# Kernel optimization log

Hardware: AMD Instinct MI355X
Metric: run time of the kernel (lower is better)

The kernel has to match this reference:

```python
import jax, jax.numpy as jnp
import numpy as np

NUM_HEADS = 16
HEAD_DIM = 128
VALUE_HEAD_DIM = 128
CHUNK = 1024
ROPE_BASE = 10000.0


def _rope(q, k, start):
    # q, k: (B, T, H, D). Rotate pairs (first half, second half) per RotaryEmbedding.
    B, T, H, D = q.shape
    half = D // 2
    inv_freq = jnp.exp(jnp.arange(half, dtype=jnp.float32) * (-np.log(ROPE_BASE) / half))
    pos = jnp.arange(T, dtype=jnp.float32) + jnp.float32(start)
    ang = pos[:, None] * inv_freq[None, :]            # (T, half)
    cos = jnp.cos(ang)[None, :, None, :].astype(q.dtype)
    sin = jnp.sin(ang)[None, :, None, :].astype(q.dtype)

    def rot(x):
        a, b = jnp.split(x, 2, axis=-1)
        return jnp.concatenate([a * cos - b * sin, b * cos + a * sin], axis=-1)

    return rot(q), rot(k)


def setup_inputs() -> dict:
    key = jax.random.key(0)
    k1, k2, k3 = jax.random.split(key, 3)
    B, L = 4, 4096
    q = jax.random.normal(k1, (B, L, NUM_HEADS, HEAD_DIM), dtype=jnp.float32)
    k = jax.random.normal(k2, (B, L, NUM_HEADS, HEAD_DIM), dtype=jnp.float32)
    v = jax.random.normal(k3, (B, L, NUM_HEADS, VALUE_HEAD_DIM), dtype=jnp.float32)
    return {"q": q, "k": k, "v": v, "start_index": 0}


def reference(q, k, v, start_index):
    # ChunkedSelfAttention.forward with cache=None, attn_mask=None, training=False:
    # RoPE at absolute positions, then causal SDPA within each chunk of size CHUNK.
    B, L, H, Dh = q.shape
    Dv = v.shape[-1]
    q, k = _rope(q, k, start_index)
    nc = L // CHUNK
    qc = q.reshape(B, nc, CHUNK, H, Dh)
    kc = k.reshape(B, nc, CHUNK, H, Dh)
    vc = v.reshape(B, nc, CHUNK, H, Dv)
    scale = 1.0 / np.sqrt(Dh).astype(np.float32)
    scores = jnp.einsum('bnqhd,bnkhd->bnhqk', qc, kc) * scale  # (B, nc, H, C, C)
    i = jnp.arange(CHUNK)
    causal = i[:, None] >= i[None, :]                          # (C, C)
    neg = jnp.asarray(jnp.finfo(scores.dtype).min, scores.dtype)
    scores = jnp.where(causal[None, None, None], scores, neg)
    attn = jax.nn.softmax(scores, axis=-1)
    out = jnp.einsum('bnhqk,bnkhd->bnqhd', attn, vc)
    return out.reshape(B, L, H, Dv)
```

## Files before the change

kernel.cpp:

```cpp
#include <hip/hip_runtime.h>


typedef __attribute__((ext_vector_type(2)))  float     f32x2;
typedef __attribute__((ext_vector_type(4)))  float     f32x4;
typedef __attribute__((ext_vector_type(16))) float     f32x16;
typedef __attribute__((ext_vector_type(8)))  _Float16  f16x8;
typedef unsigned int   u32;
typedef unsigned short u16;
typedef __attribute__((ext_vector_type(4))) unsigned int u32x4;

#define MFMA(a, b, c) __builtin_amdgcn_mfma_f32_32x32x16_f16(a, b, c, 0, 0, 0)

constexpr int Ll = 4096;
constexpr float QSCALE = 0.08838834764831845f * 1.4426950408889634f;

#define KSTR 66
#define VSTR 34
#define KBUF (64 * KSTR)
#define VBUF (128 * VSTR)
#define STG  (KBUF + VBUF)

__device__ __forceinline__ f32x4 ld_f32x4(const void* p) { f32x4 v; __builtin_memcpy(&v, p, 16); return v; }
__device__ __forceinline__ f32x2 ld_f32x2(const void* p) { f32x2 v; __builtin_memcpy(&v, p, 8);  return v; }
__device__ __forceinline__ f16x8 ld_frag(const u32* dwp) {
  f16x8 v;
  __builtin_memcpy(&v, dwp, 8);
  __builtin_memcpy(((char*)&v) + 8, dwp + 2, 8);
  return v;
}

__device__ __forceinline__ u32 packh(_Float16 a, _Float16 b) {
  return (u32)__builtin_bit_cast(u16, a) | ((u32)__builtin_bit_cast(u16, b) << 16);
}

__global__ void rope_table_k(const int* __restrict__ startp, float* __restrict__ tab) {
  int idx = blockIdx.x * 256 + threadIdx.x;
  int t = idx >> 6, hid = idx & 63;
  float a = (float)hid * (-0.14391156831212878f);
  float invf = expf(a);
  float ang = (float)(t + startp[0]) * invf;
  tab[2 * idx]     = cosf(ang);
  tab[2 * idx + 1] = sinf(ang);
}

__global__ __launch_bounds__(512, 2)
void chunked_attn_k(const float* __restrict__ Qg, const float* __restrict__ Kg,
                    const float* __restrict__ Vg, float* __restrict__ Og,
                    const float* __restrict__ tab) {
  __shared__ __align__(16) u32 lds[2 * STG];

  const int bx  = blockIdx.x;
  const int h   = bx & 15;
  const int p   = (bx >> 4) & 1;
  const int c   = (bx >> 5) & 3;
  const int b   = bx >> 7;
  const int tid = threadIdx.x;
  const int w   = tid >> 6;
  const int lane= tid & 63;
  const int l31 = lane & 31;
  const int lg2 = lane >> 5;

  const size_t cbase = (size_t)(b * Ll + c * 1024);
  const size_t hoff  = (size_t)h * 128;
  const int tb = c * 1024;

  f32x2 pk[8], pva[4], pvb[4];

  auto issue = [&](int j) {
    const float* kb_ = Kg + (cbase + (size_t)j * 64) * 2048 + hoff;
    const float* vb_ = Vg + (cbase + (size_t)j * 64) * 2048 + hoff;
    #pragma unroll
    for (int r = 0; r < 8; ++r)
      pk[r] = ld_f32x2(kb_ + (size_t)(8 * w + r) * 2048 + 2 * lane);
    #pragma unroll
    for (int rp = 0; rp < 4; ++rp) {
      const float* vr = vb_ + (size_t)(8 * w + 2 * rp) * 2048 + 2 * lane;
      pva[rp] = ld_f32x2(vr);
      pvb[rp] = ld_f32x2(vr + 2048);
    }
  };

  auto xform = [&](int j, int s) {
    u32* KB = lds + s * STG;
    u32* VB = KB + KBUF;
    const float* tbase = tab + (size_t)(tb + j * 64) * 128 + 4 * l31;
    f32x4 cs[8];
    #pragma unroll
    for (int r = 0; r < 8; ++r)
      cs[r] = ld_f32x4(tbase + (size_t)(8 * w + r) * 128);
    const float sgn = (lane < 32) ? -1.0f : 1.0f;
    #pragma unroll
    for (int r = 0; r < 8; ++r) {
      float a0 = pk[r].x, a1 = pk[r].y;
      float p0 = __shfl_xor(a0, 32), p1 = __shfl_xor(a1, 32);
      float o0 = a0 * cs[r].x + sgn * (p0 * cs[r].y);
      float o1 = a1 * cs[r].z + sgn * (p1 * cs[r].w);
      KB[(8 * w + r) * KSTR + lane] = packh((_Float16)o0, (_Float16)o1);
    }
    #pragma unroll
    for (int rp = 0; rp < 4; ++rp) {
      int kp = 4 * w + rp;
      VB[(2 * lane) * VSTR + kp]     = packh((_Float16)pva[rp].x, (_Float16)pvb[rp].x);
      VB[(2 * lane + 1) * VSTR + kp] = packh((_Float16)pva[rp].y, (_Float16)pvb[rp].y);
    }
  };

  #pragma unroll 1
  for (int sp = 0; sp < 2; ++sp) {
    const int qs = sp ? p : (3 - p);
    const int qrow = qs * 256 + w * 32 + l31;

    const float* qbase = Qg + (cbase + qrow) * 2048 + hoff;
    float xq[8][8];
    #pragma unroll
    for (int ds = 0; ds < 8; ++ds) {
      const float* ptr = qbase + ds * 16 + lg2 * 8;
      f32x4 v0 = ld_f32x4(ptr);
      f32x4 v1 = ld_f32x4(ptr + 4);
      xq[ds][0]=v0.x; xq[ds][1]=v0.y; xq[ds][2]=v0.z; xq[ds][3]=v0.w;
      xq[ds][4]=v1.x; xq[ds][5]=v1.y; xq[ds][6]=v1.z; xq[ds][7]=v1.w;
    }
    const float* trowq = tab + (size_t)(tb + qrow) * 128 + lg2 * 16;
    #pragma unroll
    for (int ds = 0; ds < 4; ++ds) {
      #pragma unroll
      for (int i2 = 0; i2 < 4; ++i2) {
        f32x4 cs = ld_f32x4(trowq + ds * 32 + i2 * 4);
        int i0 = 2 * i2;
        float a0 = xq[ds][i0],     b0 = xq[ds + 4][i0];
        xq[ds][i0]     = a0 * cs.x - b0 * cs.y;
        xq[ds + 4][i0] = b0 * cs.x + a0 * cs.y;
        float a1 = xq[ds][i0 + 1], b1 = xq[ds + 4][i0 + 1];
        xq[ds][i0 + 1]     = a1 * cs.z - b1 * cs.w;
        xq[ds + 4][i0 + 1] = b1 * cs.z + a1 * cs.w;
      }
    }
    f16x8 qh[8];
    #pragma unroll
    for (int ds = 0; ds < 8; ++ds)
      #pragma unroll
      for (int i = 0; i < 8; ++i)
        qh[ds][i] = (_Float16)(xq[ds][i] * QSCALE);

    f32x16 O[4];
    #pragma unroll
    for (int n = 0; n < 4; ++n) O[n] = (f32x16)0.0f;
    float m2 = -1e30f, lsum = 0.0f;
    const int  nt    = 4 * (qs + 1);
    const int  jmaxw = 4 * qs + (w >> 1);
    const bool oddw  = w & 1;

    issue(0);
    xform(0, 0);
    __syncthreads();

    for (int j = 0; j < nt; ++j) {
      const int s = j & 1;
      const bool more = (j + 1 < nt);
      if (more) issue(j + 1);

      if (j <= jmaxw) {
        const bool full = oddw || (j < jmaxw);
        const u32* KB = lds + s * STG;
        const u32* VB = KB + KBUF;
        const u32* kr0 = KB + (size_t)l31 * KSTR + lg2 * 4;
        const u32* kr1 = kr0 + (size_t)32 * KSTR;

        f32x16 S0 = (f32x16)0.0f, S1 = (f32x16)0.0f;
        __builtin_amdgcn_s_setprio(1);
        #pragma unroll
        for (int ds = 0; ds < 8; ++ds) {
          S0 = MFMA(ld_frag(kr0 + ds * 8), qh[ds], S0);
          if (full) S1 = MFMA(ld_frag(kr1 + ds * 8), qh[ds], S1);
        }
        __builtin_amdgcn_s_setprio(0);

        if (j == jmaxw) {
          #pragma unroll
          for (int r = 0; r < 16; ++r) {
            int crow = (r & 3) + 8 * (r >> 2) + 4 * lg2;
            if (crow > l31) { if (oddw) S1[r] = -1e30f; else S0[r] = -1e30f; }
          }
        }

        float tm = S0[0];
        #pragma unroll
        for (int r = 1; r < 16; ++r) tm = fmaxf(tm, S0[r]);
        if (full) {
          #pragma unroll
          for (int r = 0; r < 16; ++r) tm = fmaxf(tm, S1[r]);
        }
        tm = fmaxf(tm, __shfl_xor(tm, 32));
        if (!__all(tm <= m2 + 8.0f)) {
          float m2n = fmaxf(m2, tm);
          float fac = exp2f(m2 - m2n);
          lsum *= fac;
          #pragma unroll
          for (int r = 0; r < 16; ++r) {
            int rq = (r & 3) + 8 * (r >> 2) + 4 * lg2;
            float fr = __shfl(fac, rq);
            O[0][r] *= fr; O[1][r] *= fr; O[2][r] *= fr; O[3][r] *= fr;
          }
          m2 = m2n;
        }
        u32 U[16];
        float ps = 0.0f;
        #pragma unroll
        for (int t = 0; t < 8; ++t) {
          float e0 = exp2f(S0[2 * t]     - m2);
          float e1 = exp2f(S0[2 * t + 1] - m2);
          U[t] = packh((_Float16)e0, (_Float16)e1);
          ps += e0 + e1;
        }
        if (full) {
          #pragma unroll
          for (int t = 0; t < 8; ++t) {
            float e0 = exp2f(S1[2 * t]     - m2);
            float e1 = exp2f(S1[2 * t + 1] - m2);
            U[8 + t] = packh((_Float16)e0, (_Float16)e1);
            ps += e0 + e1;
          }
        }
        ps += __shfl_xor(ps, 32);
        lsum += ps;

        __builtin_amdgcn_s_setprio(1);
        #pragma unroll
        for (int ks = 0; ks < 4; ++ks) {
          if (ks >= 2 && !full) continue;
          u32 a0 = U[4 * ks + 0], a1 = U[4 * ks + 1];
          u32 b0 = U[4 * ks + 2], b1 = U[4 * ks + 3];
          asm("v_permlane32_swap_b32 %0, %1" : "+v"(a0), "+v"(b0));
          asm("v_permlane32_swap_b32 %0, %1" : "+v"(a1), "+v"(b1));
          u32x4 t4; t4.x = a0; t4.y = a1; t4.z = b0; t4.w = b1;
          f16x8 pa = __builtin_bit_cast(f16x8, t4);
          #pragma unroll
          for (int n = 0; n < 4; ++n) {
            const u32* vp = VB + (size_t)(32 * n + l31) * VSTR + 8 * ks + 4 * lg2;
            O[n] = MFMA(pa, ld_frag(vp), O[n]);
          }
        }
        __builtin_amdgcn_s_setprio(0);
      }

      if (more) xform(j + 1, s ^ 1);
      __syncthreads();
    }

    float inv = 1.0f / lsum;
    #pragma unroll
    for (int r = 0; r < 16; ++r) {
      int rq = (r & 3) + 8 * (r >> 2) + 4 * lg2;
      float fi = __shfl(inv, rq);
      float* orow = Og + (cbase + qs * 256 + w * 32 + rq) * 2048 + hoff + l31;
      orow[0]  = O[0][r] * fi;
      orow[32] = O[1][r] * fi;
      orow[64] = O[2][r] * fi;
      orow[96] = O[3][r] * fi;
    }
  }
}

extern "C" void kernel_launch(void* const* d_in, const int* in_sizes, int n_in,
                              void* d_out, int out_size, void* d_ws, size_t ws_size,
                              hipStream_t stream) {
  const float* q = (const float*)d_in[0];
  const float* k = (const float*)d_in[1];
  const float* v = (const float*)d_in[2];
  const int* start = (const int*)d_in[3];
  float* out = (float*)d_out;
  float* tab = (float*)d_ws;

  rope_table_k<<<dim3(1024), dim3(256), 0, stream>>>(start, tab);
  chunked_attn_k<<<dim3(512), dim3(512), 0, stream>>>(q, k, v, out, tab);
}
```

Measured before the change: 315.7 us.

## Precompute RoPE'd fp16 K and transposed fp16 V in separate prep kernels

Adds two prepass kernels. One applies RoPE to K and converts it to fp16 in a swizzled per-chunk tile layout, and the other converts V to fp16 and transposes it into tiles. The attention kernel then streams these pre-formatted tiles straight into LDS with 16-byte copies and uses XOR swizzle addressing instead of padded strides. The aim is to halve K/V bytes read inside the main loop and remove per-tile rotary and transpose work that attention blocks repeat. In exchange it adds extra kernel launches and a full write and re-read of 128 MB of workspace, and it falls back to the old kernel if the workspace is too small.

```diff
diff --git a/kernel.cpp b/kernel.cpp
--- a/kernel.cpp
+++ b/kernel.cpp
@@ -14,21 +14,17 @@
 constexpr int Ll = 4096;
 constexpr float QSCALE = 0.08838834764831845f * 1.4426950408889634f;
 
-#define KSTR 66
-#define VSTR 34
-#define KBUF (64 * KSTR)
-#define VBUF (128 * VSTR)
-#define STG  (KBUF + VBUF)
-
 __device__ __forceinline__ f32x4 ld_f32x4(const void* p) { f32x4 v; __builtin_memcpy(&v, p, 16); return v; }
 __device__ __forceinline__ f32x2 ld_f32x2(const void* p) { f32x2 v; __builtin_memcpy(&v, p, 8);  return v; }
+__device__ __forceinline__ u32x4 ld_u32x4(const void* p) { u32x4 v; __builtin_memcpy(&v, p, 16); return v; }
+__device__ __forceinline__ void  st_u32x4(void* p, u32x4 v) { __builtin_memcpy(p, &v, 16); }
+__device__ __forceinline__ f16x8 ld_f16x8(const void* p) { f16x8 v; __builtin_memcpy(&v, p, 16); return v; }
 __device__ __forceinline__ f16x8 ld_frag(const u32* dwp) {
   f16x8 v;
   __builtin_memcpy(&v, dwp, 8);
   __builtin_memcpy(((char*)&v) + 8, dwp + 2, 8);
   return v;
 }
-
 __device__ __forceinline__ u32 packh(_Float16 a, _Float16 b) {
   return (u32)__builtin_bit_cast(u16, a) | ((u32)__builtin_bit_cast(u16, b) << 16);
 }
@@ -43,11 +39,67 @@
   tab[2 * idx + 1] = sinf(ang);
 }
 
+__global__ __launch_bounds__(256)
+void prep_k_kernel(const float* __restrict__ Kg, const float* __restrict__ tab,
+                   u32* __restrict__ Kh) {
+  const int R    = blockIdx.x * 4 + (threadIdx.x >> 6);
+  const int lane = threadIdx.x & 63;
+  const int h  = R & 15;
+  const int bt = R >> 4;
+  const int b  = bt >> 12;
+  const int t  = bt & 4095;
+  const int c  = t >> 10;
+  const int j  = (t >> 6) & 15;
+  const int row = t & 63;
+  const int GID = (b * 4 + c) * 16 + h;
+  const int sw  = (row & 7) << 4;
+  const int dc  = ((4 * lane) ^ sw) >> 1;
+  f32x2 a = ld_f32x2(Kg + (size_t)R * 128 + dc);
+  float p0 = __shfl_xor(a.x, 32);
+  float p1 = __shfl_xor(a.y, 32);
+  f32x4 cs = ld_f32x4(tab + (size_t)t * 128 + 2 * (dc & 63));
+  const float sgn = (dc < 64) ? -1.0f : 1.0f;
+  float o0 = a.x * cs.x + sgn * (p0 * cs.y);
+  float o1 = a.y * cs.z + sgn * (p1 * cs.w);
+  Kh[((size_t)(GID * 16 + j) * 64 + row) * 64 + lane] = packh((_Float16)o0, (_Float16)o1);
+}
+
+__global__ __launch_bounds__(256)
+void prep_vt_kernel(const float* __restrict__ Vg, u32* __restrict__ VT) {
+  __shared__ __align__(16) u32 tile[4096];
+  const int gj  = blockIdx.x;
+  const int GID = gj >> 4, j = gj & 15;
+  const int h = GID & 15, c = (GID >> 4) & 3, b = GID >> 6;
+  const int tid = threadIdx.x;
+  const size_t rowbase = ((size_t)(b * 4096 + c * 1024 + j * 64)) * 16 + h;
+  const int k  = tid >> 2;
+  const int dq = tid & 3;
+  u16* t16 = (u16*)tile;
+  #pragma unroll
+  for (int it = 0; it < 8; ++it) {
+    int dv0 = dq * 4 + 16 * it;
+    f32x4 v4 = ld_f32x4(Vg + (rowbase + (size_t)k * 16) * 128 + dv0);
+    #pragma unroll
+    for (int u = 0; u < 4; ++u) {
+      int dv = dv0 + u;
+      int ci = k ^ ((dv & 7) << 3);
+      t16[dv * 64 + ci] = __builtin_bit_cast(u16, (_Float16)v4[u]);
+    }
+  }
+  __syncthreads();
+  const u32* tsrc = tile + 16 * tid;
+  u32* dst = VT + (size_t)gj * 4096 + 16 * tid;
+  #pragma unroll
+  for (int u = 0; u < 4; ++u) st_u32x4(dst + 4 * u, ld_u32x4(tsrc + 4 * u));
+}
+
+#define ATT_STG 8192
+
 __global__ __launch_bounds__(512, 2)
-void chunked_attn_k(const float* __restrict__ Qg, const float* __restrict__ Kg,
-                    const float* __restrict__ Vg, float* __restrict__ Og,
-                    const float* __restrict__ tab) {
-  __shared__ __align__(16) u32 lds[2 * STG];
+void attn_f16_k(const float* __restrict__ Qg, const u32* __restrict__ Kh,
+                const u32* __restrict__ VT, float* __restrict__ Og,
+                const float* __restrict__ tab) {
+  __shared__ __align__(16) u32 lds[2 * ATT_STG];
 
   const int bx  = blockIdx.x;
   const int h   = bx & 15;
@@ -62,46 +114,27 @@
 
   const size_t cbase = (size_t)(b * Ll + c * 1024);
   const size_t hoff  = (size_t)h * 128;
-  const int tb = c * 1024;
-
-  f32x2 pk[8], pva[4], pvb[4];
-
+  const int tb  = c * 1024;
+  const int GID = (b * 4 + c) * 16 + h;
+  const u32* khg = Kh + (size_t)GID * 16 * 4096;
+  const u32* vtg = VT + (size_t)GID * 16 * 4096;
+
+  u32x4 stg[4];
   auto issue = [&](int j) {
-    const float* kb_ = Kg + (cbase + (size_t)j * 64) * 2048 + hoff;
-    const float* vb_ = Vg + (cbase + (size_t)j * 64) * 2048 + hoff;
-    #pragma unroll
-    for (int r = 0; r < 8; ++r)
-      pk[r] = ld_f32x2(kb_ + (size_t)(8 * w + r) * 2048 + 2 * lane);
-    #pragma unroll
-    for (int rp = 0; rp < 4; ++rp) {
-      const float* vr = vb_ + (size_t)(8 * w + 2 * rp) * 2048 + 2 * lane;
-      pva[rp] = ld_f32x2(vr);
-      pvb[rp] = ld_f32x2(vr + 2048);
+    #pragma unroll
+    for (int i = 0; i < 4; ++i) {
+      int ch = w + 8 * i;
+      const u32* src = (ch < 16) ? (khg + (size_t)j * 4096 + ch * 256 + 4 * lane)
+                                 : (vtg + (size_t)j * 4096 + (ch - 16) * 256 + 4 * lane);
+      stg[i] = ld_u32x4(src);
     }
   };
-
-  auto xform = [&](int j, int s) {
-    u32* KB = lds + s * STG;
-    u32* VB = KB + KBUF;
-    const float* tbase = tab + (size_t)(tb + j * 64) * 128 + 4 * l31;
-    f32x4 cs[8];
-    #pragma unroll
-    for (int r = 0; r < 8; ++r)
-      cs[r] = ld_f32x4(tbase + (size_t)(8 * w + r) * 128);
-    const float sgn = (lane < 32) ? -1.0f : 1.0f;
-    #pragma unroll
-    for (int r = 0; r < 8; ++r) {
-      float a0 = pk[r].x, a1 = pk[r].y;
-      float p0 = __shfl_xor(a0, 32), p1 = __shfl_xor(a1, 32);
-      float o0 = a0 * cs[r].x + sgn * (p0 * cs[r].y);
-      float o1 = a1 * cs[r].z + sgn * (p1 * cs[r].w);
-      KB[(8 * w + r) * KSTR + lane] = packh((_Float16)o0, (_Float16)o1);
-    }
-    #pragma unroll
-    for (int rp = 0; rp < 4; ++rp) {
-      int kp = 4 * w + rp;
-      VB[(2 * lane) * VSTR + kp]     = packh((_Float16)pva[rp].x, (_Float16)pvb[rp].x);
-      VB[(2 * lane + 1) * VSTR + kp] = packh((_Float16)pva[rp].y, (_Float16)pvb[rp].y);
+  auto store_stage = [&](int s) {
+    u32* dst0 = lds + (size_t)s * ATT_STG;
+    #pragma unroll
+    for (int i = 0; i < 4; ++i) {
+      int ch = w + 8 * i;
+      st_u32x4(dst0 + ch * 256 + 4 * lane, stg[i]);
     }
   };
 
@@ -151,7 +184,7 @@
     const bool oddw  = w & 1;
 
     issue(0);
-    xform(0, 0);
+    store_stage(0);
     __syncthreads();
 
     for (int j = 0; j < nt; ++j) {
@@ -161,17 +194,19 @@
 
       if (j <= jmaxw) {
         const bool full = oddw || (j < jmaxw);
-        const u32* KB = lds + s * STG;
-        const u32* VB = KB + KBUF;
-        const u32* kr0 = KB + (size_t)l31 * KSTR + lg2 * 4;
-        const u32* kr1 = kr0 + (size_t)32 * KSTR;
+        const u32* KB = lds + (size_t)s * ATT_STG;
+        const u32* VB = KB + 4096;
+        const u32* kr0 = KB + (size_t)l31 * 64;
+        const u32* kr1 = kr0 + 32 * 64;
+        const int  swk = (l31 & 7) << 2;
 
         f32x16 S0 = (f32x16)0.0f, S1 = (f32x16)0.0f;
         __builtin_amdgcn_s_setprio(1);
         #pragma unroll
         for (int ds = 0; ds < 8; ++ds) {
-          S0 = MFMA(ld_frag(kr0 + ds * 8), qh[ds], S0);
-          if (full) S1 = MFMA(ld_frag(kr1 + ds * 8), qh[ds], S1);
+          int dc = (8 * ds + 4 * lg2) ^ swk;
+          S0 = MFMA(ld_f16x8(kr0 + dc), qh[ds], S0);
+          if (full) S1 = MFMA(ld_f16x8(kr1 + dc), qh[ds], S1);
         }
         __builtin_amdgcn_s_setprio(0);
 
@@ -234,16 +269,16 @@
           asm("v_permlane32_swap_b32 %0, %1" : "+v"(a1), "+v"(b1));
           u32x4 t4; t4.x = a0; t4.y = a1; t4.z = b0; t4.w = b1;
           f16x8 pa = __builtin_bit_cast(f16x8, t4);
+          int dcv = (8 * ks + 4 * lg2) ^ swk;
           #pragma unroll
           for (int n = 0; n < 4; ++n) {
-            const u32* vp = VB + (size_t)(32 * n + l31) * VSTR + 8 * ks + 4 * lg2;
-            O[n] = MFMA(pa, ld_frag(vp), O[n]);
+            O[n] = MFMA(pa, ld_f16x8(VB + (size_t)(32 * n + l31) * 32 + dcv), O[n]);
           }
         }
         __builtin_amdgcn_s_setprio(0);
       }
 
-      if (more) xform(j + 1, s ^ 1);
+      if (more) store_stage(s ^ 1);
       __syncthreads();
     }
 
@@ -261,6 +296,230 @@
   }
 }
 
+#define KSTR 66
+#define VSTR 34
+#define KBUF (64 * KSTR)
+#define VBUF (128 * VSTR)
+#define STG  (KBUF + VBUF)
+
+__global__ __launch_bounds__(512, 2)
+void chunked_attn_fb(const float* __restrict__ Qg, const float* __restrict__ Kg,
+                     const float* __restrict__ Vg, float* __restrict__ Og,
+                     const float* __restrict__ tab) {
+  __shared__ __align__(16) u32 lds[2 * STG];
+
+  const int bx  = blockIdx.x;
+  const int h   = bx & 15;
+  const int p   = (bx >> 4) & 1;
+  const int c   = (bx >> 5) & 3;
+  const int b   = bx >> 7;
+  const int tid = threadIdx.x;
+  const int w   = tid >> 6;
+  const int lane= tid & 63;
+  const int l31 = lane & 31;
+  const int lg2 = lane >> 5;
+
+  const size_t cbase = (size_t)(b * Ll + c * 1024);
+  const size_t hoff  = (size_t)h * 128;
+  const int tb = c * 1024;
+
+  f32x2 pk[8], pva[4], pvb[4];
+
+  auto issue = [&](int j) {
+    const float* kb_ = Kg + (cbase + (size_t)j * 64) * 2048 + hoff;
+    const float* vb_ = Vg + (cbase + (size_t)j * 64) * 2048 + hoff;
+    #pragma unroll
+    for (int r = 0; r < 8; ++r)
+      pk[r] = ld_f32x2(kb_ + (size_t)(8 * w + r) * 2048 + 2 * lane);
+    #pragma unroll
+    for (int rp = 0; rp < 4; ++rp) {
+      const float* vr = vb_ + (size_t)(8 * w + 2 * rp) * 2048 + 2 * lane;
+      pva[rp] = ld_f32x2(vr);
+      pvb[rp] = ld_f32x2(vr + 2048);
+    }
+  };
+
+  auto xform = [&](int j, int s) {
+    u32* KB = lds + s * STG;
+    u32* VB = KB + KBUF;
+    const float* tbase = tab + (size_t)(tb + j * 64) * 128 + 4 * l31;
+    f32x4 cs[8];
+    #pragma unroll
+    for (int r = 0; r < 8; ++r)
+      cs[r] = ld_f32x4(tbase + (size_t)(8 * w + r) * 128);
+    const float sgn = (lane < 32) ? -1.0f : 1.0f;
+    #pragma unroll
+    for (int r = 0; r < 8; ++r) {
+      float a0 = pk[r].x, a1 = pk[r].y;
+      float p0 = __shfl_xor(a0, 32), p1 = __shfl_xor(a1, 32);
+      float o0 = a0 * cs[r].x + sgn * (p0 * cs[r].y);
+      float o1 = a1 * cs[r].z + sgn * (p1 * cs[r].w);
+      KB[(8 * w + r) * KSTR + lane] = packh((_Float16)o0, (_Float16)o1);
+    }
+    #pragma unroll
+    for (int rp = 0; rp < 4; ++rp) {
+      int kp = 4 * w + rp;
+      VB[(2 * lane) * VSTR + kp]     = packh((_Float16)pva[rp].x, (_Float16)pvb[rp].x);
+      VB[(2 * lane + 1) * VSTR + kp] = packh((_Float16)pva[rp].y, (_Float16)pvb[rp].y);
+    }
+  };
+
+  #pragma unroll 1
+  for (int sp = 0; sp < 2; ++sp) {
+    const int qs = sp ? p : (3 - p);
+    const int qrow = qs * 256 + w * 32 + l31;
+
+    const float* qbase = Qg + (cbase + qrow) * 2048 + hoff;
+    float xq[8][8];
+    #pragma unroll
+    for (int ds = 0; ds < 8; ++ds) {
+      const float* ptr = qbase + ds * 16 + lg2 * 8;
+      f32x4 v0 = ld_f32x4(ptr);
+      f32x4 v1 = ld_f32x4(ptr + 4);
+      xq[ds][0]=v0.x; xq[ds][1]=v0.y; xq[ds][2]=v0.z; xq[ds][3]=v0.w;
+      xq[ds][4]=v1.x; xq[ds][5]=v1.y; xq[ds][6]=v1.z; xq[ds][7]=v1.w;
+    }
+    const float* trowq = tab + (size_t)(tb + qrow) * 128 + lg2 * 16;
+    #pragma unroll
+    for (int ds = 0; ds < 4; ++ds) {
+      #pragma unroll
+      for (int i2 = 0; i2 < 4; ++i2) {
+        f32x4 cs = ld_f32x4(trowq + ds * 32 + i2 * 4);
+        int i0 = 2 * i2;
+        float a0 = xq[ds][i0],     b0 = xq[ds + 4][i0];
+        xq[ds][i0]     = a0 * cs.x - b0 * cs.y;
+        xq[ds + 4][i0] = b0 * cs.x + a0 * cs.y;
+        float a1 = xq[ds][i0 + 1], b1 = xq[ds + 4][i0 + 1];
+        xq[ds][i0 + 1]     = a1 * cs.z - b1 * cs.w;
+        xq[ds + 4][i0 + 1] = b1 * cs.z + a1 * cs.w;
+      }
+    }
+    f16x8 qh[8];
+    #pragma unroll
+    for (int ds = 0; ds < 8; ++ds)
+      #pragma unroll
+      for (int i = 0; i < 8; ++i)
+        qh[ds][i] = (_Float16)(xq[ds][i] * QSCALE);
+
+    f32x16 O[4];
+    #pragma unroll
+    for (int n = 0; n < 4; ++n) O[n] = (f32x16)0.0f;
+    float m2 = -1e30f, lsum = 0.0f;
+    const int  nt    = 4 * (qs + 1);
+    const int  jmaxw = 4 * qs + (w >> 1);
+    const bool oddw  = w & 1;
+
+    issue(0);
+    xform(0, 0);
+    __syncthreads();
+
+    for (int j = 0; j < nt; ++j) {
+      const int s = j & 1;
+      const bool more = (j + 1 < nt);
+      if (more) issue(j + 1);
+
+      if (j <= jmaxw) {
+        const bool full = oddw || (j < jmaxw);
+        const u32* KB = lds + s * STG;
+        const u32* VB = KB + KBUF;
+        const u32* kr0 = KB + (size_t)l31 * KSTR + lg2 * 4;
+        const u32* kr1 = kr0 + (size_t)32 * KSTR;
+
+        f32x16 S0 = (f32x16)0.0f, S1 = (f32x16)0.0f;
+        __builtin_amdgcn_s_setprio(1);
+        #pragma unroll
+        for (int ds = 0; ds < 8; ++ds) {
+          S0 = MFMA(ld_frag(kr0 + ds * 8), qh[ds], S0);
+          if (full) S1 = MFMA(ld_frag(kr1 + ds * 8), qh[ds], S1);
+        }
+        __builtin_amdgcn_s_setprio(0);
+
+        if (j == jmaxw) {
+          #pragma unroll
+          for (int r = 0; r < 16; ++r) {
+            int crow = (r & 3) + 8 * (r >> 2) + 4 * lg2;
+            if (crow > l31) { if (oddw) S1[r] = -1e30f; else S0[r] = -1e30f; }
+          }
+        }
+
+        float tm = S0[0];
+        #pragma unroll
+        for (int r = 1; r < 16; ++r) tm = fmaxf(tm, S0[r]);
+        if (full) {
+          #pragma unroll
+          for (int r = 0; r < 16; ++r) tm = fmaxf(tm, S1[r]);
+        }
+        tm = fmaxf(tm, __shfl_xor(tm, 32));
+        if (!__all(tm <= m2 + 8.0f)) {
+          float m2n = fmaxf(m2, tm);
+          float fac = exp2f(m2 - m2n);
+          lsum *= fac;
+          #pragma unroll
+          for (int r = 0; r < 16; ++r) {
+            int rq = (r & 3) + 8 * (r >> 2) + 4 * lg2;
+            float fr = __shfl(fac, rq);
+            O[0][r] *= fr; O[1][r] *= fr; O[2][r] *= fr; O[3][r] *= fr;
+          }
+          m2 = m2n;
+        }
+        u32 U[16];
+        float ps = 0.0f;
+        #pragma unroll
+        for (int t = 0; t < 8; ++t) {
+          float e0 = exp2f(S0[2 * t]     - m2);
+          float e1 = exp2f(S0[2 * t + 1] - m2);
+          U[t] = packh((_Float16)e0, (_Float16)e1);
+          ps += e0 + e1;
+        }
+        if (full) {
+          #pragma unroll
+          for (int t = 0; t < 8; ++t) {
+            float e0 = exp2f(S1[2 * t]     - m2);
+            float e1 = exp2f(S1[2 * t + 1] - m2);
+            U[8 + t] = packh((_Float16)e0, (_Float16)e1);
+            ps += e0 + e1;
+          }
+        }
+        ps += __shfl_xor(ps, 32);
+        lsum += ps;
+
+        __builtin_amdgcn_s_setprio(1);
+        #pragma unroll
+        for (int ks = 0; ks < 4; ++ks) {
+          if (ks >= 2 && !full) continue;
+          u32 a0 = U[4 * ks + 0], a1 = U[4 * ks + 1];
+          u32 b0 = U[4 * ks + 2], b1 = U[4 * ks + 3];
+          asm("v_permlane32_swap_b32 %0, %1" : "+v"(a0), "+v"(b0));
+          asm("v_permlane32_swap_b32 %0, %1" : "+v"(a1), "+v"(b1));
+          u32x4 t4; t4.x = a0; t4.y = a1; t4.z = b0; t4.w = b1;
+          f16x8 pa = __builtin_bit_cast(f16x8, t4);
+          #pragma unroll
+          for (int n = 0; n < 4; ++n) {
+            const u32* vp = VB + (size_t)(32 * n + l31) * VSTR + 8 * ks + 4 * lg2;
+            O[n] = MFMA(pa, ld_frag(vp), O[n]);
+          }
+        }
+        __builtin_amdgcn_s_setprio(0);
+      }
+
+      if (more) xform(j + 1, s ^ 1);
+      __syncthreads();
+    }
+
+    float inv = 1.0f / lsum;
+    #pragma unroll
+    for (int r = 0; r < 16; ++r) {
+      int rq = (r & 3) + 8 * (r >> 2) + 4 * lg2;
+      float fi = __shfl(inv, rq);
+      float* orow = Og + (cbase + qs * 256 + w * 32 + rq) * 2048 + hoff + l31;
+      orow[0]  = O[0][r] * fi;
+      orow[32] = O[1][r] * fi;
+      orow[64] = O[2][r] * fi;
+      orow[96] = O[3][r] * fi;
+    }
+  }
+}
+
 extern "C" void kernel_launch(void* const* d_in, const int* in_sizes, int n_in,
                               void* d_out, int out_size, void* d_ws, size_t ws_size,
                               hipStream_t stream) {
@@ -269,8 +528,21 @@
   const float* v = (const float*)d_in[2];
   const int* start = (const int*)d_in[3];
   float* out = (float*)d_out;
+
   float* tab = (float*)d_ws;
+  const size_t KH_OFFB = 2u * 1024 * 1024;
+  const size_t VT_OFFB = KH_OFFB + 64u * 1024 * 1024;
+  const size_t NEED = VT_OFFB + 64u * 1024 * 1024;
 
   rope_table_k<<<dim3(1024), dim3(256), 0, stream>>>(start, tab);
-  chunked_attn_k<<<dim3(512), dim3(512), 0, stream>>>(q, k, v, out, tab);
-}
+
+  if (ws_size >= NEED) {
+    u32* Kh = (u32*)((char*)d_ws + KH_OFFB);
+    u32* VT = (u32*)((char*)d_ws + VT_OFFB);
+    prep_k_kernel<<<dim3(65536), dim3(256), 0, stream>>>(k, tab, Kh);
+    prep_vt_kernel<<<dim3(4096), dim3(256), 0, stream>>>(v, VT);
+    attn_f16_k<<<dim3(512), dim3(512), 0, stream>>>(q, Kh, VT, out, tab);
+  } else {
+    chunked_attn_fb<<<dim3(512), dim3(512), 0, stream>>>(q, k, v, out, tab);
+  }
+}
```

New measurement: 273.5 us. 1.15x faster.
